# Kernel tuning notes

Hardware: AMD Instinct MI355X
Metric: run time of the kernel (lower is better)

The kernel has to match this reference:

```python
import jax, jax.numpy as jnp
import numpy as np

N = 65536  # number of points
# (out_ch, in_ch) for the 8 shared-MLP (1x1-conv) blocks
_DIMS = [(64, 3), (64, 64), (128, 64), (1024, 128), (512, 1088), (256, 512), (128, 256), (1, 128)]


def setup_inputs() -> dict:
    key = jax.random.key(0)
    ks = jax.random.split(key, 1 + 2 * len(_DIMS))
    inp = {"x": jax.random.normal(ks[0], (1, 1, N, 3), jnp.float32)}
    for i, (o, c) in enumerate(_DIMS):
        scale = 1.0 / np.sqrt(c)
        inp[f"W{i+1}"] = jax.random.normal(ks[1 + 2 * i], (o, c), jnp.float32) * scale
        inp[f"b{i+1}"] = jax.random.uniform(ks[2 + 2 * i], (o,), jnp.float32, -scale, scale)
    return inp


def reference(x, W1, b1, W2, b2, W3, b3, W4, b4, W5, b5, W6, b6, W7, b7, W8, b8):
    # x: [1,1,n,3]. Conv2d with kernel [1,3] over the width-3 axis == per-point linear on xyz.
    pts = x[0, 0]                                   # [n,3]
    n = pts.shape[0]
    h = jax.nn.relu(pts @ W1.T + b1)                # [n,64]   block1
    h = jax.nn.relu(h @ W2.T + b2)                  # [n,64]   block2 (kept for skip-concat)
    y = jax.nn.relu(h @ W3.T + b3)                  # [n,128]  block3
    y = jax.nn.relu(y @ W4.T + b4)                  # [n,1024] block4
    g = jnp.max(y, axis=0)                          # [1024]   global max-pool over points
    # broadcast global feature to every point and concat with per-point features -> [n,1088]
    feat = jnp.concatenate([h, jnp.broadcast_to(g, (n, g.shape[0]))], axis=1)
    z = jax.nn.relu(feat @ W5.T + b5)               # [n,512]
    z = jax.nn.relu(z @ W6.T + b6)                  # [n,256]
    z = jax.nn.relu(z @ W7.T + b7)                  # [n,128]
    z = z @ W8.T + b8                               # [n,1]    block8 (no relu)
    return z.reshape(1, 1, n, 1)
```

## Files before the change

### kernel.cpp

```cpp
#include <hip/hip_runtime.h>

#define NPTS 65536

typedef __bf16 bf16_t;
typedef __bf16 bf16x8 __attribute__((ext_vector_type(8)));
typedef float f32x16 __attribute__((ext_vector_type(16)));

#define MFMA32(A, B, C) __builtin_amdgcn_mfma_f32_32x32x16_bf16(A, B, C, 0, 0, 0)

__device__ __forceinline__ float relu(float v) { return v > 0.f ? v : 0.f; }


struct PrepSeg { const float* src; bf16_t* h; bf16_t* l; int SW; int K; int nblk; };
struct PrepAll { PrepSeg seg[6]; };

__global__ __launch_bounds__(256, 2) void kprep_k1a(
    PrepAll pa,
    const float* __restrict__ x, const float* __restrict__ W1, const float* __restrict__ b1,
    bf16_t* __restrict__ h1h, bf16_t* __restrict__ h1l) {
  if (blockIdx.x < 166) {
    int blk = blockIdx.x, i = 0;
    while (blk >= pa.seg[i].nblk) { blk -= pa.seg[i].nblk; ++i; }
    const PrepSeg sg = pa.seg[i];
    int t8 = blk * 256 + threadIdx.x;
    int l = t8 & 63;
    int rest = t8 >> 6;
    int NKC = sg.K >> 4;
    int kc = rest % NKC, st = rest / NKC;
    int n = st * 32 + (l & 31);
    int k0 = kc * 16 + (l >> 5) * 8;
    const float* src = sg.src + (size_t)n * sg.SW + k0;
    bf16x8 hv, lv;
#pragma unroll
    for (int j = 0; j < 8; ++j) {
      float v = src[j];
      bf16_t h = (bf16_t)v;
      hv[j] = h; lv[j] = (bf16_t)(v - (float)h);
    }
    *(bf16x8*)(sg.h + (size_t)t8 * 8) = hv;
    *(bf16x8*)(sg.l + (size_t)t8 * 8) = lv;
  } else {
    int p = (blockIdx.x - 166) * 256 + threadIdx.x;
    float x0 = x[p * 3 + 0], x1 = x[p * 3 + 1], x2 = x[p * 3 + 2];
    int b = p >> 7, mi = (p >> 5) & 3, p31 = p & 31;
#pragma unroll
    for (int kc = 0; kc < 4; ++kc)
#pragma unroll
      for (int hbw = 0; hbw < 2; ++hbw) {
        bf16x8 hv, lv;
#pragma unroll
        for (int j = 0; j < 8; ++j) {
          int c = kc * 16 + hbw * 8 + j;
          float v = relu(fmaf(W1[c * 3], x0, fmaf(W1[c * 3 + 1], x1, fmaf(W1[c * 3 + 2], x2, b1[c]))));
          bf16_t h = (bf16_t)v;
          hv[j] = h; lv[j] = (bf16_t)(v - (float)h);
        }
        size_t off = (((size_t)(b * 4 + kc) * 4 + mi) * 64 + hbw * 32 + p31) * 8;
        *(bf16x8*)(h1h + off) = hv;
        *(bf16x8*)(h1l + off) = lv;
      }
  }
}

struct Oct { bf16x8 h0, l0, h1, l1; };
__device__ __forceinline__ Oct epi_pack(const f32x16& accv, int hb) {
  float a[16], rcv[8];
#pragma unroll
  for (int r = 0; r < 16; ++r) a[r] = relu(accv[r]);
#pragma unroll
  for (int j = 0; j < 8; ++j) rcv[j] = __shfl_xor(hb ? a[j] : a[8 + j], 32);
  float o0[8], o1[8];
#pragma unroll
  for (int j = 0; j < 4; ++j) {
    o0[j]     = hb ? rcv[j]     : a[j];
    o0[4 + j] = hb ? a[8 + j]   : rcv[j];
    o1[j]     = hb ? rcv[4 + j] : a[4 + j];
    o1[4 + j] = hb ? a[12 + j]  : rcv[4 + j];
  }
  Oct o;
#pragma unroll
  for (int j = 0; j < 8; ++j) {
    bf16_t x0 = (bf16_t)o0[j]; o.h0[j] = x0; o.l0[j] = (bf16_t)(o0[j] - (float)x0);
    bf16_t x1 = (bf16_t)o1[j]; o.h1[j] = x1; o.l1[j] = (bf16_t)(o1[j] - (float)x1);
  }
  return o;
}

__device__ __forceinline__ void epi_store_lds(const Oct& o, bf16_t* H, bf16_t* L, int ob, int p31) {
  *(bf16x8*)(H + (ob + p31) * 8)      = o.h0;
  *(bf16x8*)(H + (ob + 32 + p31) * 8) = o.h1;
  *(bf16x8*)(L + (ob + p31) * 8)      = o.l0;
  *(bf16x8*)(L + (ob + 32 + p31) * 8) = o.l1;
}

__device__ __forceinline__ void binit2(f32x16 acc[2], const float* bias, int base, int hb) {
#pragma unroll
  for (int r = 0; r < 16; ++r) {
    float bv = bias[base + 8 * (r >> 2) + 4 * hb + (r & 3)];
    acc[0][r] = bv; acc[1][r] = bv;
  }
}

template <int PB, int K, int MODE>
__global__ __launch_bounds__(256, 3) void gemmS(
    const bf16_t* __restrict__ Ah, const bf16_t* __restrict__ Al,
    const bf16_t* __restrict__ Wh, const bf16_t* __restrict__ Wl,
    const float* __restrict__ bias, int nko,
    bf16_t* __restrict__ Oh, bf16_t* __restrict__ Ol,
    float* __restrict__ aux, const float* __restrict__ w8, const float* __restrict__ b8) {
  constexpr int WC = 4 / PB;
  constexpr int NKC = K / 16;
  constexpr int KG = 2;
  constexpr int NG = NKC / KG;
  __shared__ bf16_t smem[2][PB][2][KG * 2048];

  int tid = threadIdx.x;
  int lane = tid & 63;
  int w = __builtin_amdgcn_readfirstlane(tid >> 6);
  int rg = w / WC, cw = w % WC;
  int hb = lane >> 5, p31 = lane & 31;
  int bx = blockIdx.x;
  int st0 = blockIdx.y * WC + cw;
  int bblk = bx * PB + rg;

  f32x16 acc[4];
#pragma unroll
  for (int r = 0; r < 16; ++r) {
    float bv = bias[st0 * 32 + 8 * (r >> 2) + 4 * hb + (r & 3)];
#pragma unroll
    for (int mi = 0; mi < 4; ++mi) acc[mi][r] = bv;
  }

  auto stage = [&](int buf, int g) {
#pragma unroll
    for (int i = 0; i < PB * 4; ++i) {
      int u = i * 256 + tid;
      int rgs = u >> 10, rem = u & 1023;
      int t = rem >> 9, inner = rem & 511;
      const bf16_t* src = (t ? Al : Ah) +
          ((size_t)(bx * PB + rgs) * NKC + g * KG) * 2048 + inner * 8;
      *(bf16x8*)&smem[buf][rgs][t][inner * 8] = *(const bf16x8*)src;
    }
  };

  bf16x8 wch[KG], wcl[KG], wnh[KG], wnl[KG];
  auto wload = [&](int g, bf16x8* h, bf16x8* l) {
#pragma unroll
    for (int kcl = 0; kcl < KG; ++kcl) {
      size_t wo = (((size_t)st0 * NKC + g * KG + kcl) * 64 + lane) * 8;
      h[kcl] = *(const bf16x8*)(Wh + wo);
      l[kcl] = *(const bf16x8*)(Wl + wo);
    }
  };

  auto compute = [&](int buf, bf16x8* h, bf16x8* l) {
#pragma unroll
    for (int kcl = 0; kcl < KG; ++kcl)
#pragma unroll
      for (int mi = 0; mi < 4; ++mi) {
        const bf16_t* xp = &smem[buf][rg][0][((kcl * 4 + mi) * 64 + lane) * 8];
        bf16x8 xh = *(const bf16x8*)xp;
        bf16x8 xl = *(const bf16x8*)(xp + KG * 2048);
        acc[mi] = MFMA32(h[kcl], xh, acc[mi]);
        acc[mi] = MFMA32(l[kcl], xh, acc[mi]);
        acc[mi] = MFMA32(h[kcl], xl, acc[mi]);
      }
  };

  stage(0, 0);
  wload(0, wch, wcl);
  for (int g = 0; g < NG; ++g) {
    __syncthreads();
    if (g + 1 < NG) {
      stage((g + 1) & 1, g + 1);
      wload(g + 1, wnh, wnl);
    }
    compute(g & 1, wch, wcl);
#pragma unroll
    for (int kcl = 0; kcl < KG; ++kcl) { wch[kcl] = wnh[kcl]; wcl[kcl] = wnl[kcl]; }
  }

  if constexpr (MODE == 0) {
#pragma unroll
    for (int mi = 0; mi < 4; ++mi) {
      Oct o = epi_pack(acc[mi], hb);
      int kco = st0 * 2 + hb;
      size_t ob = ((size_t)(bblk * nko + kco) * 4 + mi) * 64;
      *(bf16x8*)(Oh + (ob + p31) * 8)      = o.h0;
      *(bf16x8*)(Ol + (ob + p31) * 8)      = o.l0;
      *(bf16x8*)(Oh + (ob + 32 + p31) * 8) = o.h1;
      *(bf16x8*)(Ol + (ob + 32 + p31) * 8) = o.l1;
    }
  } else if constexpr (MODE == 1) {
#pragma unroll
    for (int r = 0; r < 16; ++r) {
      float m = relu(acc[0][r]);
#pragma unroll
      for (int mi = 1; mi < 4; ++mi) m = fmaxf(m, relu(acc[mi][r]));
#pragma unroll
      for (int off = 1; off < 32; off <<= 1) m = fmaxf(m, __shfl_xor(m, off));
      if (p31 == 0)
        aux[(size_t)bx * 1024 + st0 * 32 + 8 * (r >> 2) + 4 * hb + (r & 3)] = m;
    }
  } else {
    __shared__ float sp[4][128];
    float w8v[16];
#pragma unroll
    for (int r = 0; r < 16; ++r) w8v[r] = w8[st0 * 32 + 8 * (r >> 2) + 4 * hb + (r & 3)];
#pragma unroll
    for (int mi = 0; mi < 4; ++mi) {
      float s = 0.f;
#pragma unroll
      for (int r = 0; r < 16; ++r) s = fmaf(relu(acc[mi][r]), w8v[r], s);
      s += __shfl_xor(s, 32);
      if (hb == 0) sp[w][mi * 32 + p31] = s;
    }
    __syncthreads();
    if (tid < 128)
      aux[(size_t)bx * 128 + tid] = sp[0][tid] + sp[1][tid] + sp[2][tid] + sp[3][tid] + b8[0];
  }
}

__global__ __launch_bounds__(512, 1) void kl34max(
    const bf16_t* __restrict__ h2h, const bf16_t* __restrict__ h2l,
    const bf16_t* __restrict__ W3h, const bf16_t* __restrict__ W3l,
    const float* __restrict__ b3,
    const bf16_t* __restrict__ Wh, const bf16_t* __restrict__ Wl,
    const float* __restrict__ bias, float* __restrict__ gpart) {
  __shared__ __align__(16) bf16_t sA[81920];
  bf16_t* wq = sA + 65536;
  int tid = threadIdx.x, lane = tid & 63;
  int w = __builtin_amdgcn_readfirstlane(tid >> 6);
  int w3 = w & 3, t = w >> 2;
  int hb = lane >> 5, p31 = lane & 31;
  int bx = blockIdx.x;
  int pb = bx * 2 + t;
  int rot = (bx >> 2) & 7;
  bf16_t* sT = sA + t * 32768;
  bf16_t* wbuf = wq + w * 2048;

  {
    bf16x8 hx[4], lx[4];
#pragma unroll
    for (int kc = 0; kc < 4; ++kc) {
      size_t so = (((size_t)(pb * 4 + kc) * 4 + w3) * 64 + lane) * 8;
      hx[kc] = *(const bf16x8*)(h2h + so);
      lx[kc] = *(const bf16x8*)(h2l + so);
    }
#pragma unroll
    for (int spr = 0; spr < 2; ++spr) {
      f32x16 a3[2];
#pragma unroll
      for (int s = 0; s < 2; ++s) {
        int st = spr * 2 + s;
#pragma unroll
        for (int r = 0; r < 16; ++r)
          a3[s][r] = b3[st * 32 + 8 * (r >> 2) + 4 * hb + (r & 3)];
      }
#pragma unroll
      for (int kc = 0; kc < 4; ++kc)
#pragma unroll
        for (int s = 0; s < 2; ++s) {
          int st = spr * 2 + s;
          size_t wo = ((size_t)(st * 4 + kc) * 64 + lane) * 8;
          bf16x8 wh3 = *(const bf16x8*)(W3h + wo);
          bf16x8 wl3 = *(const bf16x8*)(W3l + wo);
          a3[s] = MFMA32(wh3, hx[kc], a3[s]);
          a3[s] = MFMA32(wl3, hx[kc], a3[s]);
          a3[s] = MFMA32(wh3, lx[kc], a3[s]);
        }
#pragma unroll
      for (int s = 0; s < 2; ++s) {
        int st = spr * 2 + s;
        Oct o = epi_pack(a3[s], hb);
        epi_store_lds(o, sT, sT + 16384, ((st * 2 + hb) * 4 + w3) * 64, p31);
      }
    }
  }
  __syncthreads();

  auto issueW = [&](int u) {
    int jj = u >> 3, kc = u & 7;
    int st = ((jj + rot) & 7) * 4 + w3;
    const bf16_t* gph = Wh + ((size_t)(st * 8 + kc) * 64 + lane) * 8;
    const bf16_t* gpl = Wl + ((size_t)(st * 8 + kc) * 64 + lane) * 8;
    bf16_t* lp = wbuf + (u & 1) * 1024;
    __builtin_amdgcn_global_load_lds(
        (const __attribute__((address_space(1))) void*)gph,
        (__attribute__((address_space(3))) void*)lp, 16, 0, 0);
    __builtin_amdgcn_global_load_lds(
        (const __attribute__((address_space(1))) void*)gpl,
        (__attribute__((address_space(3))) void*)(lp + 512), 16, 0, 0);
  };
  issueW(0);

  f32x16 acc[4];
#pragma unroll 1
  for (int u = 0; u < 64; ++u) {
    if (u + 1 < 64) {
      issueW(u + 1);
      asm volatile("s_waitcnt vmcnt(2)" ::: "memory");
    } else {
      asm volatile("s_waitcnt vmcnt(0)" ::: "memory");
    }
    __builtin_amdgcn_sched_barrier(0);
    int jj = u >> 3, kc = u & 7;
    int st = ((jj + rot) & 7) * 4 + w3;
    if (kc == 0) {
#pragma unroll
      for (int r = 0; r < 16; ++r) {
        float bv = bias[st * 32 + 8 * (r >> 2) + 4 * hb + (r & 3)];
#pragma unroll
        for (int mi = 0; mi < 4; ++mi) acc[mi][r] = bv;
      }
    }
    const bf16_t* wb = wbuf + (u & 1) * 1024;
    bf16x8 cwh = *(const bf16x8*)(wb + lane * 8);
    bf16x8 cwl = *(const bf16x8*)(wb + 512 + lane * 8);
    __builtin_amdgcn_s_setprio(1);
#pragma unroll
    for (int mi = 0; mi < 4; ++mi) {
      const bf16_t* xp = sT + ((kc * 4 + mi) * 64 + lane) * 8;
      bf16x8 xh = *(const bf16x8*)xp;
      bf16x8 xl = *(const bf16x8*)(xp + 16384);
      acc[mi] = MFMA32(cwh, xh, acc[mi]);
      acc[mi] = MFMA32(cwl, xh, acc[mi]);
      acc[mi] = MFMA32(cwh, xl, acc[mi]);
    }
    __builtin_amdgcn_s_setprio(0);
    if (kc == 7) {
#pragma unroll
      for (int r = 0; r < 16; ++r) {
        float m = fmaxf(fmaxf(acc[0][r], acc[1][r]), fmaxf(acc[2][r], acc[3][r]));
        m = fmaxf(m, 0.f);
#pragma unroll
        for (int off = 1; off < 32; off <<= 1) m = fmaxf(m, __shfl_xor(m, off));
        if (p31 == 0)
          gpart[(size_t)pb * 1024 + st * 32 + 8 * (r >> 2) + 4 * hb + (r & 3)] = m;
      }
    }
  }
}

__global__ __launch_bounds__(256) void kgmax(const float* __restrict__ gpart, float* __restrict__ g) {
  int t = blockIdx.x * 256 + threadIdx.x;
  int c = t & 1023, rg = t >> 10;
  const float* gp = gpart + (size_t)rg * 64 * 1024 + c;
  float m = 0.f;
#pragma unroll 8
  for (int r = 0; r < 64; ++r) m = fmaxf(m, gp[(size_t)r * 1024]);
  atomicMax((unsigned int*)(g + c), __float_as_uint(m));
}

__global__ __launch_bounds__(256) void kc5(
    const float* __restrict__ W5, const float* __restrict__ b5,
    const float* __restrict__ g, float* __restrict__ c5) {
  int lane = threadIdx.x & 63;
  int wv = blockIdx.x * 4 + (threadIdx.x >> 6);
  float gv[16];
#pragma unroll
  for (int k = 0; k < 16; ++k) gv[k] = g[k * 64 + lane];
#pragma unroll
  for (int i = 0; i < 4; ++i) {
    int c = wv * 4 + i;
    const float* wrow = W5 + (size_t)c * 1088 + 64;
    float acc = 0.f;
#pragma unroll
    for (int k = 0; k < 16; ++k) acc = fmaf(wrow[k * 64 + lane], gv[k], acc);
#pragma unroll
    for (int off = 1; off < 64; off <<= 1) acc += __shfl_xor(acc, off);
    if (lane == 0) c5[c] = acc + b5[c];
  }
}


__global__ __launch_bounds__(256, 2) void mega2(
    const bf16_t* __restrict__ h2gh, const bf16_t* __restrict__ h2gl,
    const bf16_t* __restrict__ W5h, const bf16_t* __restrict__ W5l, const float* __restrict__ c5,
    const bf16_t* __restrict__ W6h, const bf16_t* __restrict__ W6l, const float* __restrict__ b6,
    const bf16_t* __restrict__ W7h, const bf16_t* __restrict__ W7l, const float* __restrict__ b7,
    const float* __restrict__ w8, const float* __restrict__ b8v, float* __restrict__ out) {
  __shared__ __align__(16) bf16_t smem[32768];
  __shared__ float sp[4][64];
  int tid = threadIdx.x, lane = tid & 63;
  int w = __builtin_amdgcn_readfirstlane(tid >> 6);
  int hb = lane >> 5, p31 = lane & 31;
  int b = blockIdx.x;
  int B = b >> 1, half = b & 1;

  bf16x8 xh[4][2], xl[4][2];
#pragma unroll
  for (int kc = 0; kc < 4; ++kc)
#pragma unroll
    for (int mi = 0; mi < 2; ++mi) {
      size_t so = (((size_t)((B * 4 + kc) * 4 + half * 2 + mi)) * 64 + lane) * 8;
      xh[kc][mi] = *(const bf16x8*)(h2gh + so);
      xl[kc][mi] = *(const bf16x8*)(h2gl + so);
    }

  f32x16 z6a[2][2];
#pragma unroll
  for (int s = 0; s < 2; ++s)
#pragma unroll
    for (int r = 0; r < 16; ++r) {
      float bv = b6[(w * 2 + s) * 32 + 8 * (r >> 2) + 4 * hb + (r & 3)];
      z6a[s][0][r] = bv; z6a[s][1][r] = bv;
    }

  bf16x8 w5h[4], w5l[4];
  auto w5load = [&](int g) {
#pragma unroll
    for (int kc = 0; kc < 4; ++kc) {
      size_t wo = (((size_t)(g * 4 + w) * 4 + kc) * 64 + lane) * 8;
      w5h[kc] = *(const bf16x8*)(W5h + wo);
      w5l[kc] = *(const bf16x8*)(W5l + wo);
    }
  };
  w5load(0);

  bf16x8 cwh[2], cwl[2], nwh[2], nwl[2];
  auto w6load = [&](int g, int kc, bf16x8* hh, bf16x8* ll) {
#pragma unroll
    for (int s = 0; s < 2; ++s) {
      size_t wo = ((size_t)((w * 2 + s) * 32 + g * 8 + kc) * 64 + lane) * 8;
      hh[s] = *(const bf16x8*)(W6h + wo);
      ll[s] = *(const bf16x8*)(W6l + wo);
    }
  };

  for (int g5 = 0; g5 < 4; ++g5) {
    bf16_t* zbuf = smem + (g5 & 1) * 16384;
    int st5 = g5 * 4 + w;
    f32x16 a5[2];
    binit2(a5, c5, st5 * 32, hb);
    __builtin_amdgcn_s_setprio(1);
#pragma unroll
    for (int kc = 0; kc < 4; ++kc) {
#pragma unroll
      for (int mi = 0; mi < 2; ++mi) a5[mi] = MFMA32(w5h[kc], xh[kc][mi], a5[mi]);
#pragma unroll
      for (int mi = 0; mi < 2; ++mi) a5[mi] = MFMA32(w5l[kc], xh[kc][mi], a5[mi]);
#pragma unroll
      for (int mi = 0; mi < 2; ++mi) a5[mi] = MFMA32(w5h[kc], xl[kc][mi], a5[mi]);
    }
    __builtin_amdgcn_s_setprio(0);
    if (g5 < 3) w5load(g5 + 1);
#pragma unroll
    for (int mi = 0; mi < 2; ++mi) {
      Oct o = epi_pack(a5[mi], hb);
      epi_store_lds(o, zbuf, zbuf + 8192, ((w * 2 + hb) * 2 + mi) * 64, p31);
    }
    w6load(g5, 0, cwh, cwl);
    __syncthreads();
#pragma unroll
    for (int kc = 0; kc < 8; ++kc) {
      if (kc < 7) w6load(g5, kc + 1, nwh, nwl);
      bf16x8 zxh[2], zxl[2];
#pragma unroll
      for (int mi = 0; mi < 2; ++mi) {
        const bf16_t* xp = zbuf + ((kc * 2 + mi) * 64 + lane) * 8;
        zxh[mi] = *(const bf16x8*)xp;
        zxl[mi] = *(const bf16x8*)(xp + 8192);
      }
      __builtin_amdgcn_s_setprio(1);
#pragma unroll
      for (int s = 0; s < 2; ++s)
#pragma unroll
        for (int mi = 0; mi < 2; ++mi) z6a[s][mi] = MFMA32(cwh[s], zxh[mi], z6a[s][mi]);
#pragma unroll
      for (int s = 0; s < 2; ++s)
#pragma unroll
        for (int mi = 0; mi < 2; ++mi) z6a[s][mi] = MFMA32(cwl[s], zxh[mi], z6a[s][mi]);
#pragma unroll
      for (int s = 0; s < 2; ++s)
#pragma unroll
        for (int mi = 0; mi < 2; ++mi) z6a[s][mi] = MFMA32(cwh[s], zxl[mi], z6a[s][mi]);
      __builtin_amdgcn_s_setprio(0);
#pragma unroll
      for (int s = 0; s < 2; ++s) { cwh[s] = nwh[s]; cwl[s] = nwl[s]; }
    }
  }
  __syncthreads();
#pragma unroll
  for (int s = 0; s < 2; ++s) {
    int kcb = (w * 2 + s) * 2 + hb;
#pragma unroll
    for (int mi = 0; mi < 2; ++mi) {
      Oct o = epi_pack(z6a[s][mi], hb);
      epi_store_lds(o, smem, smem + 16384, (kcb * 2 + mi) * 64, p31);
    }
  }
  bf16x8 a7wh, a7wl, n7h, n7l;
  {
    size_t wo = ((size_t)(w * 16) * 64 + lane) * 8;
    a7wh = *(const bf16x8*)(W7h + wo);
    a7wl = *(const bf16x8*)(W7l + wo);
  }
  __syncthreads();
  f32x16 a7[2];
  binit2(a7, b7, w * 32, hb);
#pragma unroll
  for (int kc = 0; kc < 16; ++kc) {
    if (kc < 15) {
      size_t wo = ((size_t)(w * 16 + kc + 1) * 64 + lane) * 8;
      n7h = *(const bf16x8*)(W7h + wo);
      n7l = *(const bf16x8*)(W7l + wo);
    }
    bf16x8 zxh[2], zxl[2];
#pragma unroll
    for (int mi = 0; mi < 2; ++mi) {
      const bf16_t* xp = smem + ((kc * 2 + mi) * 64 + lane) * 8;
      zxh[mi] = *(const bf16x8*)xp;
      zxl[mi] = *(const bf16x8*)(xp + 16384);
    }
    __builtin_amdgcn_s_setprio(1);
#pragma unroll
    for (int mi = 0; mi < 2; ++mi) a7[mi] = MFMA32(a7wh, zxh[mi], a7[mi]);
#pragma unroll
    for (int mi = 0; mi < 2; ++mi) a7[mi] = MFMA32(a7wl, zxh[mi], a7[mi]);
#pragma unroll
    for (int mi = 0; mi < 2; ++mi) a7[mi] = MFMA32(a7wh, zxl[mi], a7[mi]);
    __builtin_amdgcn_s_setprio(0);
    a7wh = n7h; a7wl = n7l;
  }
  float w8v[16];
#pragma unroll
  for (int r = 0; r < 16; ++r) w8v[r] = w8[w * 32 + 8 * (r >> 2) + 4 * hb + (r & 3)];
#pragma unroll
  for (int mi = 0; mi < 2; ++mi) {
    float s = 0.f;
#pragma unroll
    for (int r = 0; r < 16; ++r) s = fmaf(relu(a7[mi][r]), w8v[r], s);
    s += __shfl_xor(s, 32);
    if (hb == 0) sp[w][mi * 32 + p31] = s;
  }
  __syncthreads();
  if (tid < 64)
    out[b * 64 + tid] = sp[0][tid] + sp[1][tid] + sp[2][tid] + sp[3][tid] + b8v[0];
}

extern "C" void kernel_launch(void* const* d_in, const int* in_sizes, int n_in,
                              void* d_out, int out_size, void* d_ws, size_t ws_size,
                              hipStream_t stream) {
  const float* x  = (const float*)d_in[0];
  const float* W1 = (const float*)d_in[1];  const float* b1 = (const float*)d_in[2];
  const float* W2 = (const float*)d_in[3];  const float* b2 = (const float*)d_in[4];
  const float* W3 = (const float*)d_in[5];  const float* b3 = (const float*)d_in[6];
  const float* W4 = (const float*)d_in[7];  const float* b4 = (const float*)d_in[8];
  const float* W5 = (const float*)d_in[9];  const float* b5 = (const float*)d_in[10];
  const float* W6 = (const float*)d_in[11]; const float* b6 = (const float*)d_in[12];
  const float* W7 = (const float*)d_in[13]; const float* b7 = (const float*)d_in[14];
  const float* W8 = (const float*)d_in[15]; const float* b8 = (const float*)d_in[16];
  float* out = (float*)d_out;

  const size_t MB = 1ull << 20;
  char* ws = (char*)d_ws;
  bf16_t* h2h = (bf16_t*)(ws + 128 * MB);  bf16_t* h2l = (bf16_t*)(ws + 136 * MB);
  bf16_t* h1h = (bf16_t*)(ws + 144 * MB);  bf16_t* h1l = (bf16_t*)(ws + 152 * MB);
  float* gpart = (float*)(ws + 208 * MB);
  float* g     = (float*)(ws + 210 * MB);
  float* c5    = (float*)(ws + 210 * MB + 4096);
  char* wb = ws + 210 * MB + 65536;
  bf16_t* W2h = (bf16_t*)(wb);             bf16_t* W2l = (bf16_t*)(wb + 8192);
  bf16_t* W3h = (bf16_t*)(wb + 16384);     bf16_t* W3l = (bf16_t*)(wb + 32768);
  bf16_t* W4h = (bf16_t*)(wb + 49152);     bf16_t* W4l = (bf16_t*)(wb + 311296);
  bf16_t* W5h = (bf16_t*)(wb + 573440);    bf16_t* W5l = (bf16_t*)(wb + 638976);
  bf16_t* W6h = (bf16_t*)(wb + 704512);    bf16_t* W6l = (bf16_t*)(wb + 966656);
  bf16_t* W7h = (bf16_t*)(wb + 1228800);   bf16_t* W7l = (bf16_t*)(wb + 1294336);

  hipMemsetAsync(g, 0, 1024 * sizeof(float), stream);

  PrepAll pa;
  pa.seg[0] = {W2, W2h, W2l, 64, 64, 2};
  pa.seg[1] = {W3, W3h, W3l, 64, 64, 4};
  pa.seg[2] = {W4, W4h, W4l, 128, 128, 64};
  pa.seg[3] = {W5, W5h, W5l, 1088, 64, 16};
  pa.seg[4] = {W6, W6h, W6l, 512, 512, 64};
  pa.seg[5] = {W7, W7h, W7l, 256, 256, 16};

  kprep_k1a<<<422, 256, 0, stream>>>(pa, x, W1, b1, h1h, h1l);
  gemmS<2, 64, 0><<<dim3(256, 1), 256, 0, stream>>>(
      h1h, h1l, W2h, W2l, b2, 4, h2h, h2l, nullptr, nullptr, nullptr);
  kl34max<<<256, 512, 0, stream>>>(h2h, h2l, W3h, W3l, b3, W4h, W4l, b4, gpart);
  kgmax<<<32, 256, 0, stream>>>(gpart, g);
  kc5<<<32, 256, 0, stream>>>(W5, b5, g, c5);
  mega2<<<1024, 256, 0, stream>>>(h2h, h2l, W5h, W5l, c5, W6h, W6l, b6,
                                  W7h, W7l, b7, W8, b8, out);
}
```

Baseline: 249.8 us.

## Share W4 tile loads across point-tile waves via block-wide LDS staging

The layer-4 weight stream used to be loaded per wave, so the two waves sharing a channel slot (one per point tile) each fetched the same W4 tile. Each step now loads two k-chunks for all four channel slots cooperatively into a shared double buffer. Waves pick their slot's data after a block-wide barrier, which halves redundant global weight traffic and halves the loop trip count. The first weight fetch is also moved ahead of the layer-3 compute to overlap with it. In exchange, every step now needs a full vmcnt(0) wait plus an s_barrier, which adds synchronisation and may reduce the latency hiding the per-wave pipeline had.

```diff
diff --git a/kernel.cpp b/kernel.cpp
--- a/kernel.cpp
+++ b/kernel.cpp
@@ -237,7 +237,26 @@
   int pb = bx * 2 + t;
   int rot = (bx >> 2) & 7;
   bf16_t* sT = sA + t * 32768;
-  bf16_t* wbuf = wq + w * 2048;
+
+  auto issueW = [&](int u) {
+    int jj = u >> 2, kp = (u & 3) * 2;
+#pragma unroll
+    for (int i = 0; i < 2; ++i) {
+      int unit = i * 8 + w;
+      int sslot = unit & 3;
+      int q     = (unit >> 2) & 1;
+      int part  = unit >> 3;
+      int st = ((jj + rot) & 7) * 4 + sslot;
+      int kc = kp + q;
+      const bf16_t* W = part ? Wl : Wh;
+      const bf16_t* gp = W + ((size_t)(st * 8 + kc) * 64 + lane) * 8;
+      bf16_t* lp = wq + (u & 1) * 8192 + (sslot * 4 + q * 2 + part) * 512;
+      __builtin_amdgcn_global_load_lds(
+          (const __attribute__((address_space(1))) void*)gp,
+          (__attribute__((address_space(3))) void*)lp, 16, 0, 0);
+    }
+  };
+  issueW(0);
 
   {
     bf16x8 hx[4], lx[4];
@@ -279,56 +298,42 @@
   }
   __syncthreads();
 
-  auto issueW = [&](int u) {
-    int jj = u >> 3, kc = u & 7;
-    int st = ((jj + rot) & 7) * 4 + w3;
-    const bf16_t* gph = Wh + ((size_t)(st * 8 + kc) * 64 + lane) * 8;
-    const bf16_t* gpl = Wl + ((size_t)(st * 8 + kc) * 64 + lane) * 8;
-    bf16_t* lp = wbuf + (u & 1) * 1024;
-    __builtin_amdgcn_global_load_lds(
-        (const __attribute__((address_space(1))) void*)gph,
-        (__attribute__((address_space(3))) void*)lp, 16, 0, 0);
-    __builtin_amdgcn_global_load_lds(
-        (const __attribute__((address_space(1))) void*)gpl,
-        (__attribute__((address_space(3))) void*)(lp + 512), 16, 0, 0);
-  };
-  issueW(0);
-
   f32x16 acc[4];
 #pragma unroll 1
-  for (int u = 0; u < 64; ++u) {
-    if (u + 1 < 64) {
-      issueW(u + 1);
-      asm volatile("s_waitcnt vmcnt(2)" ::: "memory");
-    } else {
-      asm volatile("s_waitcnt vmcnt(0)" ::: "memory");
-    }
+  for (int u = 0; u < 32; ++u) {
+    asm volatile("s_waitcnt vmcnt(0)" ::: "memory");
     __builtin_amdgcn_sched_barrier(0);
-    int jj = u >> 3, kc = u & 7;
-    int st = ((jj + rot) & 7) * 4 + w3;
-    if (kc == 0) {
+    __builtin_amdgcn_s_barrier();
+    if (u + 1 < 32) issueW(u + 1);
+    int jj = u >> 2, kp = (u & 3) * 2;
+    int stc = ((jj + rot) & 7) * 4 + w3;
+    if ((u & 3) == 0) {
 #pragma unroll
       for (int r = 0; r < 16; ++r) {
-        float bv = bias[st * 32 + 8 * (r >> 2) + 4 * hb + (r & 3)];
+        float bv = bias[stc * 32 + 8 * (r >> 2) + 4 * hb + (r & 3)];
 #pragma unroll
         for (int mi = 0; mi < 4; ++mi) acc[mi][r] = bv;
       }
     }
-    const bf16_t* wb = wbuf + (u & 1) * 1024;
-    bf16x8 cwh = *(const bf16x8*)(wb + lane * 8);
-    bf16x8 cwl = *(const bf16x8*)(wb + 512 + lane * 8);
-    __builtin_amdgcn_s_setprio(1);
-#pragma unroll
-    for (int mi = 0; mi < 4; ++mi) {
-      const bf16_t* xp = sT + ((kc * 4 + mi) * 64 + lane) * 8;
-      bf16x8 xh = *(const bf16x8*)xp;
-      bf16x8 xl = *(const bf16x8*)(xp + 16384);
-      acc[mi] = MFMA32(cwh, xh, acc[mi]);
-      acc[mi] = MFMA32(cwl, xh, acc[mi]);
-      acc[mi] = MFMA32(cwh, xl, acc[mi]);
-    }
-    __builtin_amdgcn_s_setprio(0);
-    if (kc == 7) {
+    const bf16_t* wb = wq + (u & 1) * 8192;
+#pragma unroll
+    for (int q = 0; q < 2; ++q) {
+      int kc = kp + q;
+      bf16x8 cwh = *(const bf16x8*)(wb + (w3 * 4 + q * 2) * 512 + lane * 8);
+      bf16x8 cwl = *(const bf16x8*)(wb + (w3 * 4 + q * 2 + 1) * 512 + lane * 8);
+      __builtin_amdgcn_s_setprio(1);
+#pragma unroll
+      for (int mi = 0; mi < 4; ++mi) {
+        const bf16_t* xp = sT + ((kc * 4 + mi) * 64 + lane) * 8;
+        bf16x8 xh = *(const bf16x8*)xp;
+        bf16x8 xl = *(const bf16x8*)(xp + 16384);
+        acc[mi] = MFMA32(cwh, xh, acc[mi]);
+        acc[mi] = MFMA32(cwl, xh, acc[mi]);
+        acc[mi] = MFMA32(cwh, xl, acc[mi]);
+      }
+      __builtin_amdgcn_s_setprio(0);
+    }
+    if ((u & 3) == 3) {
 #pragma unroll
       for (int r = 0; r < 16; ++r) {
         float m = fmaxf(fmaxf(acc[0][r], acc[1][r]), fmaxf(acc[2][r], acc[3][r]));
@@ -336,7 +341,7 @@
 #pragma unroll
         for (int off = 1; off < 32; off <<= 1) m = fmaxf(m, __shfl_xor(m, off));
         if (p31 == 0)
-          gpart[(size_t)pb * 1024 + st * 32 + 8 * (r >> 2) + 4 * hb + (r & 3)] = m;
+          gpart[(size_t)pb * 1024 + stc * 32 + 8 * (r >> 2) + 4 * hb + (r & 3)] = m;
       }
     }
   }
```

Result: no change. 245.4 us (-1.7%).
